# Kernel optimization log

Hardware: AMD Instinct MI355X
Metric: run time of the kernel (lower is better)

## Reference

```python
import jax, jax.numpy as jnp
import numpy as np

B, S, T = 256, 512, 32  # batch, seq_len, tag_size (includes START=T-2, END=T-1)


def setup_inputs() -> dict:
    key = jax.random.key(0)
    k1, k2, k3, k4 = jax.random.split(key, 4)
    feats = jax.random.normal(k1, (B, S, T), dtype=jnp.float32)
    transitions = jax.random.normal(k2, (T, T), dtype=jnp.float32) * 0.1
    # prefix mask: lengths in [S//2, S] (torch code assumes contiguous valid prefix)
    lengths = jax.random.randint(k3, (B,), S // 2, S + 1)
    mask = jnp.arange(S)[None, :] < lengths[:, None]  # (B,S) bool
    tags = jax.random.randint(k4, (B, S), 0, T - 2).astype(jnp.int32)
    return {"feats": feats, "transitions": transitions, "mask": mask, "tags": tags}


def _nll_loss(feats, transitions, mask, tags):
    Bx, Sx, Tx = feats.shape
    maskf = mask.astype(feats.dtype)
    # ---- forward algorithm (log partition) ----
    # partition initialized from emissions at position 1 (positions 0,1 are special)
    part0 = feats[:, 1, :]  # (B,T)
    f_seq = jnp.swapaxes(feats[:, 2:, :], 0, 1)  # (S-2, B, T)
    m_seq = jnp.swapaxes(mask[:, 2:], 0, 1)      # (S-2, B)

    def fwd_step(partition, inp):
        f_t, m_t = inp
        # cur[b, prev, next] = feats[b,t,next] + transitions[prev,next] + partition[b,prev]
        cur = f_t[:, None, :] + transitions[None, :, :] + partition[:, :, None]
        new = jax.nn.logsumexp(cur, axis=1)  # (B,T)
        # partition frozen where mask==0 (== torch masked_scatter logic)
        return jnp.where(m_t[:, None], new, partition), None

    partition, _ = jax.lax.scan(fwd_step, part0, (f_seq, m_seq))
    forward_score = jnp.sum(jax.nn.logsumexp(partition, axis=1))

    # ---- gold score ----
    tags = jnp.where(tags == -100, 0, tags)
    emis = jnp.take_along_axis(feats, tags[..., None], axis=2)[..., 0]  # (B,S)
    tr = transitions[tags[:, :-1], tags[:, 1:]]  # (B,S-1): transition into pos t (t>=1)
    # transitions only apply for t>=2; tg_energy[0] is zeroed in the torch code
    e = emis + jnp.concatenate([jnp.zeros((Bx, 2), feats.dtype), tr[:, 1:]], axis=1)
    e = e.at[:, 0].set(0.0)
    gold_score = jnp.sum(e * maskf)
    return (forward_score - gold_score) / Bx


def _viterbi(feats, transitions, mask):
    Bx, Sx, Tx = feats.shape
    lengths = mask.astype(jnp.int32).sum(axis=1)
    part0 = feats[:, 1, :]
    f_seq = jnp.swapaxes(feats[:, 2:, :], 0, 1)
    m_seq = jnp.swapaxes(mask[:, 2:], 0, 1)

    def vit_step(partition, inp):
        f_t, m_t = inp
        cur = f_t[:, None, :] + transitions[None, :, :] + partition[:, :, None]
        new = jnp.max(cur, axis=1)
        bp = jnp.argmax(cur, axis=1).astype(jnp.int32)
        bp = jnp.where(m_t[:, None], bp, 0)  # torch masked_fill_(pad, 0)
        # NOTE: viterbi partition is updated UNconditionally in the torch code
        return new, (partition, bp)

    last_part, (hist, bps) = jax.lax.scan(vit_step, part0, (f_seq, m_seq))
    history = jnp.concatenate([hist, last_part[None]], axis=0)  # (S-1,B,T)
    hist_bt = jnp.swapaxes(history, 0, 1)                        # (B,S-1,T)
    idx = jnp.broadcast_to((lengths - 2)[:, None, None], (Bx, 1, Tx))
    last_partition = jnp.take_along_axis(hist_bt, idx, axis=1)[:, 0, :]  # (B,T)
    pointer = jnp.argmax(last_partition, axis=1).astype(jnp.int32)

    def back_step(ptr, bp_t):
        new = jnp.take_along_axis(bp_t, ptr[:, None], axis=1)[:, 0]
        return new, new

    _, ptrs = jax.lax.scan(back_step, pointer, bps, reverse=True)  # (S-2,B)
    # decode_idx[0] is uninitialized in the torch code; we define it as 0
    decode = jnp.concatenate(
        [jnp.zeros((1, Bx), jnp.int32), ptrs, pointer[None, :]], axis=0
    )  # (S,B)
    path_score = jnp.zeros((Bx,), feats.dtype)  # torch returns zeros
    return path_score, decode.T


def reference(feats, transitions, mask, tags):
    loss = _nll_loss(feats, transitions, mask, tags)
    path_score, decode_idx = _viterbi(feats, transitions, mask)
    return loss, path_score, decode_idx
```

## Files before the change

kernel.cpp:

```cpp
#include <hip/hip_runtime.h>
#include <cstdint>
#include <cstddef>
#include <utility>

#define SS 512
#define TT 32
#define NB 256
#define KSTEPS 510
#define PQUADS 128

template <typename F, size_t... Is>
__device__ __forceinline__ void unroll_impl(F&& f, std::index_sequence<Is...>) {
  (f(std::integral_constant<int, (int)Is>{}), ...);
}
template <int N, typename F>
__device__ __forceinline__ void unrollN(F&& f) {
  unroll_impl(f, std::make_index_sequence<N>{});
}

template <int D>
__device__ __forceinline__ float bfly32(float v) {
  return __int_as_float(__builtin_amdgcn_ds_swizzle(__float_as_int(v), (D << 10) | 0x1f));
}
template <int D>
__device__ __forceinline__ int bfly32i(int v) {
  return __builtin_amdgcn_ds_swizzle(v, (D << 10) | 0x1f);
}

__device__ __forceinline__ float max3f(float a, float b, float c) {
  return fmaxf(fmaxf(a, b), c);
}

__device__ __forceinline__ float combine_max32(float m) {
#if __has_builtin(__builtin_amdgcn_permlane32_swap)
  auto r = __builtin_amdgcn_permlane32_swap(__float_as_uint(m), __float_as_uint(m), false, false);
  return fmaxf(__uint_as_float(r[0]), __uint_as_float(r[1]));
#else
  return fmaxf(m, __shfl_xor(m, 32, 64));
#endif
}
__device__ __forceinline__ float combine_sum32(float m) {
#if __has_builtin(__builtin_amdgcn_permlane32_swap)
  auto r = __builtin_amdgcn_permlane32_swap(__float_as_uint(m), __float_as_uint(m), false, false);
  return __uint_as_float(r[0]) + __uint_as_float(r[1]);
#else
  return m + __shfl_xor(m, 32, 64);
#endif
}

__device__ __forceinline__ int mask_mode(const void* m) {
  int w0 = ((const int*)m)[0];
  if (w0 == 1) return 0;
  if (w0 == 0x3f800000) return 2;
  return 1;
}
__device__ __forceinline__ bool mask_at(const void* m, int idx, int mode) {
  if (mode == 0) return ((const int*)m)[idx] != 0;
  if (mode == 2) return ((const float*)m)[idx] != 0.0f;
  return ((const unsigned char*)m)[idx] != 0;
}

__device__ __forceinline__ int seq_length_lane(const void* mask, int b, int lane, int mode) {
  int cnt = 0;
  for (int s = lane; s < SS; s += 64) cnt += mask_at(mask, b * SS + s, mode) ? 1 : 0;
  for (int d = 1; d < 64; d <<= 1) cnt += __shfl_xor(cnt, d, 64);
  return __builtin_amdgcn_readfirstlane(cnt);
}

__global__ __launch_bounds__(64, 1) void crf_main_kernel(
    const float* __restrict__ feats, const float* __restrict__ trans,
    const void* __restrict__ mask, const int* __restrict__ tags,
    float* __restrict__ pstore, float* __restrict__ ws_fwd,
    float* __restrict__ ws_gold, int* __restrict__ ws_ptr) {
  const int blk = blockIdx.x;
  const int tid = threadIdx.x;
  const int mode = mask_mode(mask);
  const int j = tid & 31;
  const int h = tid >> 5;

  __shared__ __align__(16) float qlds[TT];

  if (blk < NB) {
    const int b = blk;
    const int steps = seq_length_lane(mask, b, tid, mode) - 2;
    const float* fb = feats + (size_t)b * (SS * TT) + j;

    float E[16];
    unrollN<16>([&](auto I) {
      constexpr int ii = I;
      E[ii] = __expf(trans[(h * 16 + ii) * TT + j]);
    });

    float q = __expf(fb[TT]);
    int Eacc = 0;
    qlds[j] = q;
    asm volatile("" ::: "memory");
    const float4* qvh = (const float4*)qlds + h * 4;

    float fA = fb[2 * TT], fB = fb[3 * TT], fC = fb[4 * TT];
    float ef = __expf(fA);

    auto fstep = [&](int k, bool resc) {
      float4 Q0 = qvh[0], Q1 = qvh[1], Q2 = qvh[2], Q3 = qvh[3];
      int r5 = k + 5; r5 = (r5 < SS) ? r5 : (SS - 1);
      float fD = fb[r5 * TT];
      float efN = __expf(fB);
      float a0, a1, a2, a3;
      a0 = Q0.x * E[0];  a1 = Q0.y * E[1];  a2 = Q0.z * E[2];  a3 = Q0.w * E[3];
      a0 = fmaf(Q1.x, E[4], a0);  a1 = fmaf(Q1.y, E[5], a1);  a2 = fmaf(Q1.z, E[6], a2);  a3 = fmaf(Q1.w, E[7], a3);
      a0 = fmaf(Q2.x, E[8], a0);  a1 = fmaf(Q2.y, E[9], a1);  a2 = fmaf(Q2.z, E[10], a2); a3 = fmaf(Q2.w, E[11], a3);
      a0 = fmaf(Q3.x, E[12], a0); a1 = fmaf(Q3.y, E[13], a1); a2 = fmaf(Q3.z, E[14], a2); a3 = fmaf(Q3.w, E[15], a3);
      float P = (a0 + a1) + (a2 + a3);
      float Pt = combine_sum32(P);
      q = ef * Pt;
      if (resc) {
        int qb = __builtin_amdgcn_readfirstlane(__float_as_int(q));
        int e = (qb >> 23) & 0xff;
        Eacc += e - 127;
        q *= __int_as_float((254 - e) << 23);
      }
      qlds[j] = q;
      asm volatile("" ::: "memory");
      fA = fB; fB = fC; fC = fD; ef = efN;
    };

    int k = 0;
    for (; k + 4 <= steps; k += 4) {
      fstep(k, false); fstep(k + 1, false); fstep(k + 2, false); fstep(k + 3, true);
    }
    for (; k < steps; ++k) fstep(k, false);

    float s = q;
    unrollN<5>([&](auto D) { constexpr int d = 1 << D; s += bfly32<d>(s); });
    if (tid == 0) ws_fwd[b] = __logf(s) + (float)Eacc * 0.69314718056f;

  } else if (blk < 2 * NB) {
    const int b = blk - NB;
    const int steps = seq_length_lane(mask, b, tid, mode) - 2;
    const float* fb = feats + (size_t)b * (SS * TT) + j;
    float* pq = pstore + (size_t)b * (PQUADS * 128) + j * 4;

    float C[16];
    unrollN<16>([&](auto I) {
      constexpr int ii = I;
      C[ii] = trans[(h * 16 + ii) * TT + j];
    });

    float p = fb[TT];
    qlds[j] = p;
    asm volatile("" ::: "memory");
    const float4* qvh = (const float4*)qlds + h * 4;

    float fA = fb[2 * TT], fB = fb[3 * TT], fC = fb[4 * TT];
    float h0 = p, h1 = 0.f, h2 = 0.f, h3 = 0.f;

    auto vstep = [&](int k, float& hslot) {
      float4 Q0 = qvh[0], Q1 = qvh[1], Q2 = qvh[2], Q3 = qvh[3];
      int r5 = k + 5; r5 = (r5 < SS) ? r5 : (SS - 1);
      float fD = fb[r5 * TT];
      float dd[16];
      unrollN<16>([&](auto I) { constexpr int ii = I; dd[ii] = fA + C[ii]; });
      float cur[16];
      cur[0] = Q0.x + dd[0];   cur[1] = Q0.y + dd[1];   cur[2] = Q0.z + dd[2];   cur[3] = Q0.w + dd[3];
      cur[4] = Q1.x + dd[4];   cur[5] = Q1.y + dd[5];   cur[6] = Q1.z + dd[6];   cur[7] = Q1.w + dd[7];
      cur[8] = Q2.x + dd[8];   cur[9] = Q2.y + dd[9];   cur[10] = Q2.z + dd[10]; cur[11] = Q2.w + dd[11];
      cur[12] = Q3.x + dd[12]; cur[13] = Q3.y + dd[13]; cur[14] = Q3.z + dd[14]; cur[15] = Q3.w + dd[15];
      float t0 = max3f(cur[0], cur[1], cur[2]);
      float t1 = max3f(cur[3], cur[4], cur[5]);
      float t2 = max3f(cur[6], cur[7], cur[8]);
      float t3 = max3f(cur[9], cur[10], cur[11]);
      float t4 = max3f(cur[12], cur[13], cur[14]);
      float m = fmaxf(max3f(t0, t1, t2), max3f(t3, t4, cur[15]));
      float pw = combine_max32(m);
      p = pw;
      qlds[j] = pw;
      asm volatile("" ::: "memory");
      hslot = pw;
      fA = fB; fB = fC; fC = fD;
    };

    auto flush = [&](int quad) {
      if (tid < 32) {
        float4 v; v.x = h0; v.y = h1; v.z = h2; v.w = h3;
        *(float4*)(pq + quad * 128) = v;
      }
    };

    int k = 0;
    for (; k + 4 <= steps; k += 4) {
      vstep(k, h1);
      vstep(k + 1, h2);
      vstep(k + 2, h3);
      flush(k >> 2);
      vstep(k + 3, h0);
    }
    if (k < steps) vstep(k, h1);
    if (k + 1 < steps) vstep(k + 1, h2);
    if (k + 2 < steps) vstep(k + 2, h3);
    flush(k >> 2);

    float v = p;
    int idx = j;
    unrollN<5>([&](auto D) {
      constexpr int d = 1 << D;
      float vo = bfly32<d>(v);
      int io = bfly32i<d>(idx);
      bool take = (vo > v) || ((vo == v) && (io < idx));
      v = take ? vo : v;
      idx = take ? io : idx;
    });
    if (tid == 0) ws_ptr[b] = idx;

  } else {
    const int b = blk - 2 * NB;
    float acc = 0.0f;
    for (int s = tid; s < SS; s += 64) {
      if (s == 0) continue;
      if (!mask_at(mask, b * SS + s, mode)) continue;
      int tg = tags[b * SS + s];
      if (tg == -100) tg = 0;
      float e = feats[((size_t)b * SS + s) * TT + tg];
      if (s >= 2) {
        int tp = tags[b * SS + s - 1];
        if (tp == -100) tp = 0;
        e += trans[tp * TT + tg];
      }
      acc += e;
    }
    for (int d = 1; d < 64; d <<= 1) acc += __shfl_xor(acc, d, 64);
    if (tid == 0) ws_gold[b] = acc;
  }
}

__global__ __launch_bounds__(512) void crf_backtrace_kernel(
    const float* __restrict__ pstore, const float* __restrict__ feats,
    const float* __restrict__ trans, const void* __restrict__ mask,
    const int* __restrict__ ws_ptr, const float* __restrict__ ws_fwd,
    const float* __restrict__ ws_gold, float* __restrict__ out) {
  __shared__ unsigned char bp[KSTEPS * TT];
  __shared__ unsigned char path[KSTEPS * TT];
  __shared__ __align__(16) float pT[16][4][TT];
  __shared__ int entries[8];

  const int b = blockIdx.x;
  const int tid = threadIdx.x;
  const int mode = mask_mode(mask);
  const int lane = tid & 63;
  float* out_decode = out + 1 + NB;

  const int steps = seq_length_lane(mask, b, lane, mode) - 2;

  if (tid == 0) out[1 + b] = 0.0f;
  if (b == 0 && tid >= 64 && tid < 128) {
    int t = tid - 64;
    float sf = 0.0f, sg = 0.0f;
    for (int r = 0; r < 4; ++r) { sf += ws_fwd[t + 64 * r]; sg += ws_gold[t + 64 * r]; }
    for (int d = 1; d < 64; d <<= 1) { sf += __shfl_xor(sf, d, 64); sg += __shfl_xor(sg, d, 64); }
    if (t == 0) out[0] = (sf - sg) / 256.0f;
  }

  {
    const int jj = tid & 31;
    const int g = tid >> 5;
    float Cc[TT];
    unrollN<TT>([&](auto I) { constexpr int ii = I; Cc[ii] = trans[ii * TT + jj]; });
    const float* pb = pstore + (size_t)b * (PQUADS * 128);
    const float* fbb = feats + (size_t)b * (SS * TT);
    for (int q = g; q < PQUADS; q += 16) {
      float4 V = *(const float4*)(pb + q * 128 + jj * 4);
      pT[g][0][jj] = V.x; pT[g][1][jj] = V.y; pT[g][2][jj] = V.z; pT[g][3][jj] = V.w;
      asm volatile("" ::: "memory");
      unrollN<4>([&](auto R) {
        constexpr int r = R;
        const int k = 4 * q + r;
        if (k < KSTEPS) {
          unsigned char bv = 0;
          if (k < steps) {
            const float4* pr = (const float4*)pT[g][r];
            float4 P0 = pr[0], P1 = pr[1], P2 = pr[2], P3 = pr[3];
            float4 P4 = pr[4], P5 = pr[5], P6 = pr[6], P7 = pr[7];
            float fj = fbb[(k + 2) * TT + jj];
            float cur[TT];
            cur[0]  = (fj + Cc[0])  + P0.x; cur[1]  = (fj + Cc[1])  + P0.y;
            cur[2]  = (fj + Cc[2])  + P0.z; cur[3]  = (fj + Cc[3])  + P0.w;
            cur[4]  = (fj + Cc[4])  + P1.x; cur[5]  = (fj + Cc[5])  + P1.y;
            cur[6]  = (fj + Cc[6])  + P1.z; cur[7]  = (fj + Cc[7])  + P1.w;
            cur[8]  = (fj + Cc[8])  + P2.x; cur[9]  = (fj + Cc[9])  + P2.y;
            cur[10] = (fj + Cc[10]) + P2.z; cur[11] = (fj + Cc[11]) + P2.w;
            cur[12] = (fj + Cc[12]) + P3.x; cur[13] = (fj + Cc[13]) + P3.y;
            cur[14] = (fj + Cc[14]) + P3.z; cur[15] = (fj + Cc[15]) + P3.w;
            cur[16] = (fj + Cc[16]) + P4.x; cur[17] = (fj + Cc[17]) + P4.y;
            cur[18] = (fj + Cc[18]) + P4.z; cur[19] = (fj + Cc[19]) + P4.w;
            cur[20] = (fj + Cc[20]) + P5.x; cur[21] = (fj + Cc[21]) + P5.y;
            cur[22] = (fj + Cc[22]) + P5.z; cur[23] = (fj + Cc[23]) + P5.w;
            cur[24] = (fj + Cc[24]) + P6.x; cur[25] = (fj + Cc[25]) + P6.y;
            cur[26] = (fj + Cc[26]) + P6.z; cur[27] = (fj + Cc[27]) + P6.w;
            cur[28] = (fj + Cc[28]) + P7.x; cur[29] = (fj + Cc[29]) + P7.y;
            cur[30] = (fj + Cc[30]) + P7.z; cur[31] = (fj + Cc[31]) + P7.w;
            float t0 = max3f(cur[0], cur[1], cur[2]);
            float t1 = max3f(cur[3], cur[4], cur[5]);
            float t2 = max3f(cur[6], cur[7], cur[8]);
            float t3 = max3f(cur[9], cur[10], cur[11]);
            float t4 = max3f(cur[12], cur[13], cur[14]);
            float t5 = max3f(cur[15], cur[16], cur[17]);
            float t6 = max3f(cur[18], cur[19], cur[20]);
            float t7 = max3f(cur[21], cur[22], cur[23]);
            float t8 = max3f(cur[24], cur[25], cur[26]);
            float t9 = max3f(cur[27], cur[28], cur[29]);
            float ta = fmaxf(cur[30], cur[31]);
            float vmax = fmaxf(fmaxf(max3f(t0, t1, t2), max3f(t3, t4, t5)),
                               fmaxf(max3f(t6, t7, t8), fmaxf(t9, ta)));
            int bi = 31;
            unrollN<TT>([&](auto I) { constexpr int ii = 31 - I; bi = (cur[ii] == vmax) ? ii : bi; });
            bv = (unsigned char)bi;
          }
          bp[k * TT + jj] = bv;
        }
      });
    }
  }
  __syncthreads();

  const int wave = tid >> 6;
  if (lane < 32) {
    const int lo = wave * 64;
    const int hi = (lo + 64 < KSTEPS) ? (lo + 64) : KSTEPS;
    int ptr = lane;
    for (int k = hi - 1; k >= lo; --k) {
      ptr = bp[k * TT + ptr];
      path[k * TT + lane] = (unsigned char)ptr;
    }
  }
  __syncthreads();

  if (tid == 0) {
    int e = ws_ptr[b];
    for (int c = 7; c >= 0; --c) {
      entries[c] = e;
      e = path[(c * 64) * TT + e];
    }
  }
  __syncthreads();

  const int s = tid;
  int val;
  if (s == 0) val = 0;
  else if (s <= KSTEPS) { int k = s - 1; val = path[k * TT + entries[k >> 6]]; }
  else val = ws_ptr[b];
  out_decode[(size_t)b * SS + s] = (float)val;
}

extern "C" void kernel_launch(void* const* d_in, const int* in_sizes, int n_in,
                              void* d_out, int out_size, void* d_ws, size_t ws_size,
                              hipStream_t stream) {
  const float* feats = (const float*)d_in[0];
  const float* trans = (const float*)d_in[1];
  const void* mask = d_in[2];
  const int* tags = (const int*)d_in[3];
  float* out = (float*)d_out;

  unsigned char* ws = (unsigned char*)d_ws;
  const size_t PST_BYTES = (size_t)NB * PQUADS * 128 * 4;
  float* pstore = (float*)ws;
  float* ws_fwd = (float*)(ws + PST_BYTES);
  float* ws_gold = (float*)(ws + PST_BYTES + 2048);
  int* ws_ptr = (int*)(ws + PST_BYTES + 4096);

  hipLaunchKernelGGL(crf_main_kernel, dim3(3 * NB), dim3(64), 0, stream,
                     feats, trans, mask, tags, pstore, ws_fwd, ws_gold, ws_ptr);
  hipLaunchKernelGGL(crf_backtrace_kernel, dim3(NB), dim3(512), 0, stream,
                     pstore, feats, trans, mask, ws_ptr, ws_fwd, ws_gold, out);
}
```

Baseline: 112.6 us.

## Replace LDS broadcast in CRF recurrences with DPP row rotations and permlane swaps

```diff
diff --git a/kernel.cpp b/kernel.cpp
--- a/kernel.cpp
+++ b/kernel.cpp
@@ -29,6 +29,16 @@
 
 __device__ __forceinline__ float max3f(float a, float b, float c) {
   return fmaxf(fmaxf(a, b), c);
+}
+
+template <int R>
+__device__ __forceinline__ float dpp_rorf(float v) {
+  return __int_as_float(__builtin_amdgcn_update_dpp(
+      0, __float_as_int(v), 0x120 + R, 0xf, 0xf, true));
+}
+template <int R>
+__device__ __forceinline__ int dpp_rori(int v) {
+  return __builtin_amdgcn_update_dpp(0, v, 0x120 + R, 0xf, 0xf, true);
 }
 
 __device__ __forceinline__ float combine_max32(float m) {
@@ -45,6 +55,15 @@
   return __uint_as_float(r[0]) + __uint_as_float(r[1]);
 #else
   return m + __shfl_xor(m, 32, 64);
+#endif
+}
+__device__ __forceinline__ float partner16(float v) {
+#if __has_builtin(__builtin_amdgcn_permlane16_swap)
+  auto r = __builtin_amdgcn_permlane16_swap(__float_as_uint(v), __float_as_uint(v), false, false);
+  float a = __uint_as_float(r[0]), b = __uint_as_float(r[1]);
+  return (__float_as_uint(a) == __float_as_uint(v)) ? b : a;
+#else
+  return __shfl_xor(v, 16, 64);
 #endif
 }
 
@@ -75,52 +94,66 @@
   const int blk = blockIdx.x;
   const int tid = threadIdx.x;
   const int mode = mask_mode(mask);
-  const int j = tid & 31;
-  const int h = tid >> 5;
-
-  __shared__ __align__(16) float qlds[TT];
+  const int lane = tid & 63;
+  const int l15 = lane & 15;
+  const int row = lane >> 4;
+  const int heldB = (row == 1 || row == 2) ? 16 : 0;
+  const int outB  = (row == 1 || row == 3) ? 16 : 0;
+  const int heldtag = l15 + heldB;
+  const int outtag  = l15 + outB;
+  const bool lower = (lane < 32);
+
+  int src15[16];
+  src15[0] = l15;
+  unrollN<15>([&](auto RR) { constexpr int r = RR + 1; src15[r] = dpp_rori<r>(l15); });
 
   if (blk < NB) {
     const int b = blk;
     const int steps = seq_length_lane(mask, b, tid, mode) - 2;
-    const float* fb = feats + (size_t)b * (SS * TT) + j;
+    const float* fb = feats + (size_t)b * (SS * TT) + outtag;
 
     float E[16];
-    unrollN<16>([&](auto I) {
-      constexpr int ii = I;
-      E[ii] = __expf(trans[(h * 16 + ii) * TT + j]);
+    unrollN<16>([&](auto RR) {
+      constexpr int r = RR;
+      E[r] = __expf(trans[(src15[r] + heldB) * TT + outtag]);
     });
 
-    float q = __expf(fb[TT]);
+    float q = __expf(feats[(size_t)b * (SS * TT) + TT + heldtag]);
     int Eacc = 0;
-    qlds[j] = q;
-    asm volatile("" ::: "memory");
-    const float4* qvh = (const float4*)qlds + h * 4;
-
     float fA = fb[2 * TT], fB = fb[3 * TT], fC = fb[4 * TT];
     float ef = __expf(fA);
 
     auto fstep = [&](int k, bool resc) {
-      float4 Q0 = qvh[0], Q1 = qvh[1], Q2 = qvh[2], Q3 = qvh[3];
       int r5 = k + 5; r5 = (r5 < SS) ? r5 : (SS - 1);
       float fD = fb[r5 * TT];
       float efN = __expf(fB);
-      float a0, a1, a2, a3;
-      a0 = Q0.x * E[0];  a1 = Q0.y * E[1];  a2 = Q0.z * E[2];  a3 = Q0.w * E[3];
-      a0 = fmaf(Q1.x, E[4], a0);  a1 = fmaf(Q1.y, E[5], a1);  a2 = fmaf(Q1.z, E[6], a2);  a3 = fmaf(Q1.w, E[7], a3);
-      a0 = fmaf(Q2.x, E[8], a0);  a1 = fmaf(Q2.y, E[9], a1);  a2 = fmaf(Q2.z, E[10], a2); a3 = fmaf(Q2.w, E[11], a3);
-      a0 = fmaf(Q3.x, E[12], a0); a1 = fmaf(Q3.y, E[13], a1); a2 = fmaf(Q3.z, E[14], a2); a3 = fmaf(Q3.w, E[15], a3);
+      float a0 = q * E[0], a1, a2, a3;
+      a1 = dpp_rorf<1>(q) * E[1];
+      a2 = dpp_rorf<2>(q) * E[2];
+      a3 = dpp_rorf<3>(q) * E[3];
+      a0 = fmaf(dpp_rorf<4>(q),  E[4],  a0);
+      a1 = fmaf(dpp_rorf<5>(q),  E[5],  a1);
+      a2 = fmaf(dpp_rorf<6>(q),  E[6],  a2);
+      a3 = fmaf(dpp_rorf<7>(q),  E[7],  a3);
+      a0 = fmaf(dpp_rorf<8>(q),  E[8],  a0);
+      a1 = fmaf(dpp_rorf<9>(q),  E[9],  a1);
+      a2 = fmaf(dpp_rorf<10>(q), E[10], a2);
+      a3 = fmaf(dpp_rorf<11>(q), E[11], a3);
+      a0 = fmaf(dpp_rorf<12>(q), E[12], a0);
+      a1 = fmaf(dpp_rorf<13>(q), E[13], a1);
+      a2 = fmaf(dpp_rorf<14>(q), E[14], a2);
+      a3 = fmaf(dpp_rorf<15>(q), E[15], a3);
       float P = (a0 + a1) + (a2 + a3);
-      float Pt = combine_sum32(P);
-      q = ef * Pt;
+      float val = ef * combine_sum32(P);
+      float par = partner16(val);
+      float qn = lower ? val : par;
       if (resc) {
-        int qb = __builtin_amdgcn_readfirstlane(__float_as_int(q));
+        int qb = __builtin_amdgcn_readfirstlane(__float_as_int(qn));
         int e = (qb >> 23) & 0xff;
         Eacc += e - 127;
-        q *= __int_as_float((254 - e) << 23);
+        qn *= __int_as_float((254 - e) << 23);
       }
-      qlds[j] = q;
-      asm volatile("" ::: "memory");
+      q = qn;
       fA = fB; fB = fC; fC = fD; ef = efN;
     };
 
@@ -137,50 +170,57 @@
   } else if (blk < 2 * NB) {
     const int b = blk - NB;
     const int steps = seq_length_lane(mask, b, tid, mode) - 2;
-    const float* fb = feats + (size_t)b * (SS * TT) + j;
-    float* pq = pstore + (size_t)b * (PQUADS * 128) + j * 4;
+    const float* fb = feats + (size_t)b * (SS * TT) + outtag;
+    float* pq = pstore + (size_t)b * (PQUADS * 128) + lane * 4;
 
     float C[16];
-    unrollN<16>([&](auto I) {
-      constexpr int ii = I;
-      C[ii] = trans[(h * 16 + ii) * TT + j];
+    unrollN<16>([&](auto RR) {
+      constexpr int r = RR;
+      C[r] = trans[(src15[r] + heldB) * TT + outtag];
     });
 
-    float p = fb[TT];
-    qlds[j] = p;
-    asm volatile("" ::: "memory");
-    const float4* qvh = (const float4*)qlds + h * 4;
-
+    float p = feats[(size_t)b * (SS * TT) + TT + heldtag];
     float fA = fb[2 * TT], fB = fb[3 * TT], fC = fb[4 * TT];
     float h0 = p, h1 = 0.f, h2 = 0.f, h3 = 0.f;
 
     auto vstep = [&](int k, float& hslot) {
-      float4 Q0 = qvh[0], Q1 = qvh[1], Q2 = qvh[2], Q3 = qvh[3];
       int r5 = k + 5; r5 = (r5 < SS) ? r5 : (SS - 1);
       float fD = fb[r5 * TT];
       float dd[16];
-      unrollN<16>([&](auto I) { constexpr int ii = I; dd[ii] = fA + C[ii]; });
+      unrollN<16>([&](auto RR) { constexpr int r = RR; dd[r] = fA + C[r]; });
       float cur[16];
-      cur[0] = Q0.x + dd[0];   cur[1] = Q0.y + dd[1];   cur[2] = Q0.z + dd[2];   cur[3] = Q0.w + dd[3];
-      cur[4] = Q1.x + dd[4];   cur[5] = Q1.y + dd[5];   cur[6] = Q1.z + dd[6];   cur[7] = Q1.w + dd[7];
-      cur[8] = Q2.x + dd[8];   cur[9] = Q2.y + dd[9];   cur[10] = Q2.z + dd[10]; cur[11] = Q2.w + dd[11];
-      cur[12] = Q3.x + dd[12]; cur[13] = Q3.y + dd[13]; cur[14] = Q3.z + dd[14]; cur[15] = Q3.w + dd[15];
+      cur[0] = p + dd[0];
+      cur[1]  = dpp_rorf<1>(p)  + dd[1];
+      cur[2]  = dpp_rorf<2>(p)  + dd[2];
+      cur[3]  = dpp_rorf<3>(p)  + dd[3];
+      cur[4]  = dpp_rorf<4>(p)  + dd[4];
+      cur[5]  = dpp_rorf<5>(p)  + dd[5];
+      cur[6]  = dpp_rorf<6>(p)  + dd[6];
+      cur[7]  = dpp_rorf<7>(p)  + dd[7];
+      cur[8]  = dpp_rorf<8>(p)  + dd[8];
+      cur[9]  = dpp_rorf<9>(p)  + dd[9];
+      cur[10] = dpp_rorf<10>(p) + dd[10];
+      cur[11] = dpp_rorf<11>(p) + dd[11];
+      cur[12] = dpp_rorf<12>(p) + dd[12];
+      cur[13] = dpp_rorf<13>(p) + dd[13];
+      cur[14] = dpp_rorf<14>(p) + dd[14];
+      cur[15] = dpp_rorf<15>(p) + dd[15];
       float t0 = max3f(cur[0], cur[1], cur[2]);
       float t1 = max3f(cur[3], cur[4], cur[5]);
       float t2 = max3f(cur[6], cur[7], cur[8]);
       float t3 = max3f(cur[9], cur[10], cur[11]);
       float t4 = max3f(cur[12], cur[13], cur[14]);
       float m = fmaxf(max3f(t0, t1, t2), max3f(t3, t4, cur[15]));
-      float pw = combine_max32(m);
+      float full = combine_max32(m);
+      float par = partner16(full);
+      float pw = lower ? full : par;
       p = pw;
-      qlds[j] = pw;
-      asm volatile("" ::: "memory");
       hslot = pw;
       fA = fB; fB = fC; fC = fD;
     };
 
     auto flush = [&](int quad) {
-      if (tid < 32) {
+      if (lane < 32) {
         float4 v; v.x = h0; v.y = h1; v.z = h2; v.w = h3;
         *(float4*)(pq + quad * 128) = v;
       }
@@ -200,7 +240,7 @@
     flush(k >> 2);
 
     float v = p;
-    int idx = j;
+    int idx = lane & 31;
     unrollN<5>([&](auto D) {
       constexpr int d = 1 << D;
       float vo = bfly32<d>(v);
```

Result: faster. 103.6 us, median of 2 (-8.0%).

## Pack two sequences per wave and replace LDS exchange with DPP rotations

Applied to the files above, without the earlier changes.

```diff
diff --git a/kernel.cpp b/kernel.cpp
--- a/kernel.cpp
+++ b/kernel.cpp
@@ -31,20 +31,23 @@
   return fmaxf(fmaxf(a, b), c);
 }
 
-__device__ __forceinline__ float combine_max32(float m) {
-#if __has_builtin(__builtin_amdgcn_permlane32_swap)
-  auto r = __builtin_amdgcn_permlane32_swap(__float_as_uint(m), __float_as_uint(m), false, false);
-  return fmaxf(__uint_as_float(r[0]), __uint_as_float(r[1]));
+template <int R>
+__device__ __forceinline__ float dpp_rorf(float v) {
+  return __int_as_float(__builtin_amdgcn_update_dpp(
+      0, __float_as_int(v), 0x120 + R, 0xf, 0xf, true));
+}
+template <int R>
+__device__ __forceinline__ int dpp_rori(int v) {
+  return __builtin_amdgcn_update_dpp(0, v, 0x120 + R, 0xf, 0xf, true);
+}
+
+__device__ __forceinline__ float partner16(float v) {
+#if __has_builtin(__builtin_amdgcn_permlane16_swap)
+  auto r = __builtin_amdgcn_permlane16_swap(__float_as_uint(v), __float_as_uint(v), false, false);
+  float a = __uint_as_float(r[0]), b = __uint_as_float(r[1]);
+  return (__float_as_uint(a) == __float_as_uint(v)) ? b : a;
 #else
-  return fmaxf(m, __shfl_xor(m, 32, 64));
-#endif
-}
-__device__ __forceinline__ float combine_sum32(float m) {
-#if __has_builtin(__builtin_amdgcn_permlane32_swap)
-  auto r = __builtin_amdgcn_permlane32_swap(__float_as_uint(m), __float_as_uint(m), false, false);
-  return __uint_as_float(r[0]) + __uint_as_float(r[1]);
-#else
-  return m + __shfl_xor(m, 32, 64);
+  return __shfl_xor(v, 16, 64);
 #endif
 }
 
@@ -58,6 +61,16 @@
   if (mode == 0) return ((const int*)m)[idx] != 0;
   if (mode == 2) return ((const float*)m)[idx] != 0.0f;
   return ((const unsigned char*)m)[idx] != 0;
+}
+
+__device__ __forceinline__ int seqlen32(const void* mask, int b, int j32, int mode) {
+  int cnt = 0;
+  unrollN<16>([&](auto T) {
+    constexpr int t = T;
+    cnt += mask_at(mask, b * SS + j32 + 32 * t, mode) ? 1 : 0;
+  });
+  unrollN<5>([&](auto D) { constexpr int d = 1 << D; cnt += bfly32i<d>(cnt); });
+  return cnt;
 }
 
 __device__ __forceinline__ int seq_length_lane(const void* mask, int b, int lane, int mode) {
@@ -75,132 +88,92 @@
   const int blk = blockIdx.x;
   const int tid = threadIdx.x;
   const int mode = mask_mode(mask);
-  const int j = tid & 31;
-  const int h = tid >> 5;
-
-  __shared__ __align__(16) float qlds[TT];
-
-  if (blk < NB) {
-    const int b = blk;
-    const int steps = seq_length_lane(mask, b, tid, mode) - 2;
-    const float* fb = feats + (size_t)b * (SS * TT) + j;
-
-    float E[16];
-    unrollN<16>([&](auto I) {
-      constexpr int ii = I;
-      E[ii] = __expf(trans[(h * 16 + ii) * TT + j]);
+  const int tag = tid & 31;
+  const int g = tid >> 5;
+  const int rowg = (tid >> 4) & 1;
+  const int sAb = rowg ? 16 : 0;
+  const int sBb = rowg ? 0 : 16;
+
+  int src15[16];
+  src15[0] = tid & 15;
+  unrollN<15>([&](auto RR) { constexpr int r = RR + 1; src15[r] = dpp_rori<r>(tid & 15); });
+
+  if (blk < 128) {
+    const int b = blk * 2 + g;
+    const int steps = seqlen32(mask, b, tag, mode) - 2;
+    int smax;
+    { int s = steps, o = __shfl_xor(s, 32, 64); s = (o > s) ? o : s;
+      smax = __builtin_amdgcn_readfirstlane(s); }
+    const float* fb = feats + (size_t)b * (SS * TT) + tag;
+    float* pq = pstore + (size_t)b * (PQUADS * 128) + tag * 4;
+
+    float CA[16], CB[16];
+    unrollN<16>([&](auto RR) {
+      constexpr int r = RR;
+      CA[r] = trans[(sAb + src15[r]) * TT + tag];
+      CB[r] = trans[(sBb + src15[r]) * TT + tag];
     });
 
-    float q = __expf(fb[TT]);
-    int Eacc = 0;
-    qlds[j] = q;
-    asm volatile("" ::: "memory");
-    const float4* qvh = (const float4*)qlds + h * 4;
-
+    float p = fb[TT];
     float fA = fb[2 * TT], fB = fb[3 * TT], fC = fb[4 * TT];
-    float ef = __expf(fA);
-
-    auto fstep = [&](int k, bool resc) {
-      float4 Q0 = qvh[0], Q1 = qvh[1], Q2 = qvh[2], Q3 = qvh[3];
+    float h0 = p, h1 = 0.f, h2 = 0.f, h3 = 0.f;
+
+    auto vstep = [&](int k, float& hslot) {
       int r5 = k + 5; r5 = (r5 < SS) ? r5 : (SS - 1);
       float fD = fb[r5 * TT];
-      float efN = __expf(fB);
-      float a0, a1, a2, a3;
-      a0 = Q0.x * E[0];  a1 = Q0.y * E[1];  a2 = Q0.z * E[2];  a3 = Q0.w * E[3];
-      a0 = fmaf(Q1.x, E[4], a0);  a1 = fmaf(Q1.y, E[5], a1);  a2 = fmaf(Q1.z, E[6], a2);  a3 = fmaf(Q1.w, E[7], a3);
-      a0 = fmaf(Q2.x, E[8], a0);  a1 = fmaf(Q2.y, E[9], a1);  a2 = fmaf(Q2.z, E[10], a2); a3 = fmaf(Q2.w, E[11], a3);
-      a0 = fmaf(Q3.x, E[12], a0); a1 = fmaf(Q3.y, E[13], a1); a2 = fmaf(Q3.z, E[14], a2); a3 = fmaf(Q3.w, E[15], a3);
-      float P = (a0 + a1) + (a2 + a3);
-      float Pt = combine_sum32(P);
-      q = ef * Pt;
-      if (resc) {
-        int qb = __builtin_amdgcn_readfirstlane(__float_as_int(q));
-        int e = (qb >> 23) & 0xff;
-        Eacc += e - 127;
-        q *= __int_as_float((254 - e) << 23);
-      }
-      qlds[j] = q;
-      asm volatile("" ::: "memory");
-      fA = fB; fB = fC; fC = fD; ef = efN;
-    };
-
-    int k = 0;
-    for (; k + 4 <= steps; k += 4) {
-      fstep(k, false); fstep(k + 1, false); fstep(k + 2, false); fstep(k + 3, true);
-    }
-    for (; k < steps; ++k) fstep(k, false);
-
-    float s = q;
-    unrollN<5>([&](auto D) { constexpr int d = 1 << D; s += bfly32<d>(s); });
-    if (tid == 0) ws_fwd[b] = __logf(s) + (float)Eacc * 0.69314718056f;
-
-  } else if (blk < 2 * NB) {
-    const int b = blk - NB;
-    const int steps = seq_length_lane(mask, b, tid, mode) - 2;
-    const float* fb = feats + (size_t)b * (SS * TT) + j;
-    float* pq = pstore + (size_t)b * (PQUADS * 128) + j * 4;
-
-    float C[16];
-    unrollN<16>([&](auto I) {
-      constexpr int ii = I;
-      C[ii] = trans[(h * 16 + ii) * TT + j];
-    });
-
-    float p = fb[TT];
-    qlds[j] = p;
-    asm volatile("" ::: "memory");
-    const float4* qvh = (const float4*)qlds + h * 4;
-
-    float fA = fb[2 * TT], fB = fb[3 * TT], fC = fb[4 * TT];
-    float h0 = p, h1 = 0.f, h2 = 0.f, h3 = 0.f;
-
-    auto vstep = [&](int k, float& hslot) {
-      float4 Q0 = qvh[0], Q1 = qvh[1], Q2 = qvh[2], Q3 = qvh[3];
-      int r5 = k + 5; r5 = (r5 < SS) ? r5 : (SS - 1);
-      float fD = fb[r5 * TT];
-      float dd[16];
-      unrollN<16>([&](auto I) { constexpr int ii = I; dd[ii] = fA + C[ii]; });
-      float cur[16];
-      cur[0] = Q0.x + dd[0];   cur[1] = Q0.y + dd[1];   cur[2] = Q0.z + dd[2];   cur[3] = Q0.w + dd[3];
-      cur[4] = Q1.x + dd[4];   cur[5] = Q1.y + dd[5];   cur[6] = Q1.z + dd[6];   cur[7] = Q1.w + dd[7];
-      cur[8] = Q2.x + dd[8];   cur[9] = Q2.y + dd[9];   cur[10] = Q2.z + dd[10]; cur[11] = Q2.w + dd[11];
-      cur[12] = Q3.x + dd[12]; cur[13] = Q3.y + dd[13]; cur[14] = Q3.z + dd[14]; cur[15] = Q3.w + dd[15];
+      float pp = partner16(p);
+      float cur[32];
+      unrollN<16>([&](auto RR) {
+        constexpr int r = RR;
+        float d = fA + CA[r];
+        if constexpr (r == 0) cur[0] = p + d;
+        else cur[r] = dpp_rorf<r>(p) + d;
+      });
+      unrollN<16>([&](auto RR) {
+        constexpr int r = RR;
+        float d = fA + CB[r];
+        if constexpr (r == 0) cur[16] = pp + d;
+        else cur[16 + r] = dpp_rorf<r>(pp) + d;
+      });
       float t0 = max3f(cur[0], cur[1], cur[2]);
       float t1 = max3f(cur[3], cur[4], cur[5]);
       float t2 = max3f(cur[6], cur[7], cur[8]);
       float t3 = max3f(cur[9], cur[10], cur[11]);
       float t4 = max3f(cur[12], cur[13], cur[14]);
-      float m = fmaxf(max3f(t0, t1, t2), max3f(t3, t4, cur[15]));
-      float pw = combine_max32(m);
+      float t5 = max3f(cur[15], cur[16], cur[17]);
+      float t6 = max3f(cur[18], cur[19], cur[20]);
+      float t7 = max3f(cur[21], cur[22], cur[23]);
+      float t8 = max3f(cur[24], cur[25], cur[26]);
+      float t9 = max3f(cur[27], cur[28], cur[29]);
+      float ta = fmaxf(cur[30], cur[31]);
+      float vmax = fmaxf(fmaxf(max3f(t0, t1, t2), max3f(t3, t4, t5)),
+                         fmaxf(max3f(t6, t7, t8), fmaxf(t9, ta)));
+      float pw = (k < steps) ? vmax : p;
       p = pw;
-      qlds[j] = pw;
-      asm volatile("" ::: "memory");
       hslot = pw;
       fA = fB; fB = fC; fC = fD;
     };
 
     auto flush = [&](int quad) {
-      if (tid < 32) {
-        float4 v; v.x = h0; v.y = h1; v.z = h2; v.w = h3;
-        *(float4*)(pq + quad * 128) = v;
-      }
+      float4 v; v.x = h0; v.y = h1; v.z = h2; v.w = h3;
+      *(float4*)(pq + quad * 128) = v;
     };
 
     int k = 0;
-    for (; k + 4 <= steps; k += 4) {
+    for (; k + 4 <= smax; k += 4) {
       vstep(k, h1);
       vstep(k + 1, h2);
       vstep(k + 2, h3);
       flush(k >> 2);
       vstep(k + 3, h0);
     }
-    if (k < steps) vstep(k, h1);
-    if (k + 1 < steps) vstep(k + 1, h2);
-    if (k + 2 < steps) vstep(k + 2, h3);
+    if (k < smax) vstep(k, h1);
+    if (k + 1 < smax) vstep(k + 1, h2);
+    if (k + 2 < smax) vstep(k + 2, h3);
     flush(k >> 2);
 
     float v = p;
-    int idx = j;
+    int idx = tag;
     unrollN<5>([&](auto D) {
       constexpr int d = 1 << D;
       float vo = bfly32<d>(v);
@@ -209,10 +182,92 @@
       v = take ? vo : v;
       idx = take ? io : idx;
     });
-    if (tid == 0) ws_ptr[b] = idx;
+    if (tag == 0) ws_ptr[b] = idx;
+
+  } else if (blk < 256) {
+    const int b = (blk - 128) * 2 + g;
+    const int steps = seqlen32(mask, b, tag, mode) - 2;
+    int smax;
+    { int s = steps, o = __shfl_xor(s, 32, 64); s = (o > s) ? o : s;
+      smax = __builtin_amdgcn_readfirstlane(s); }
+    const float* fb = feats + (size_t)b * (SS * TT) + tag;
+
+    float EA[16], EB[16];
+    unrollN<16>([&](auto RR) {
+      constexpr int r = RR;
+      EA[r] = __expf(trans[(sAb + src15[r]) * TT + tag]);
+      EB[r] = __expf(trans[(sBb + src15[r]) * TT + tag]);
+    });
+
+    float q = __expf(fb[TT]);
+    int Eacc = 0;
+    float fA = fb[2 * TT], fB = fb[3 * TT], fC = fb[4 * TT];
+    float ef = __expf(fA);
+
+    auto fstep = [&](int k, bool resc) {
+      int r5 = k + 5; r5 = (r5 < SS) ? r5 : (SS - 1);
+      float fD = fb[r5 * TT];
+      float efN = __expf(fB);
+      float pp = partner16(q);
+      float a0, a1, a2, a3;
+      a0 = q * EA[0];
+      a1 = dpp_rorf<1>(q) * EA[1];
+      a2 = dpp_rorf<2>(q) * EA[2];
+      a3 = dpp_rorf<3>(q) * EA[3];
+      a0 = fmaf(dpp_rorf<4>(q),  EA[4],  a0);
+      a1 = fmaf(dpp_rorf<5>(q),  EA[5],  a1);
+      a2 = fmaf(dpp_rorf<6>(q),  EA[6],  a2);
+      a3 = fmaf(dpp_rorf<7>(q),  EA[7],  a3);
+      a0 = fmaf(dpp_rorf<8>(q),  EA[8],  a0);
+      a1 = fmaf(dpp_rorf<9>(q),  EA[9],  a1);
+      a2 = fmaf(dpp_rorf<10>(q), EA[10], a2);
+      a3 = fmaf(dpp_rorf<11>(q), EA[11], a3);
+      a0 = fmaf(dpp_rorf<12>(q), EA[12], a0);
+      a1 = fmaf(dpp_rorf<13>(q), EA[13], a1);
+      a2 = fmaf(dpp_rorf<14>(q), EA[14], a2);
+      a3 = fmaf(dpp_rorf<15>(q), EA[15], a3);
+      a0 = fmaf(pp, EB[0], a0);
+      a1 = fmaf(dpp_rorf<1>(pp),  EB[1],  a1);
+      a2 = fmaf(dpp_rorf<2>(pp),  EB[2],  a2);
+      a3 = fmaf(dpp_rorf<3>(pp),  EB[3],  a3);
+      a0 = fmaf(dpp_rorf<4>(pp),  EB[4],  a0);
+      a1 = fmaf(dpp_rorf<5>(pp),  EB[5],  a1);
+      a2 = fmaf(dpp_rorf<6>(pp),  EB[6],  a2);
+      a3 = fmaf(dpp_rorf<7>(pp),  EB[7],  a3);
+      a0 = fmaf(dpp_rorf<8>(pp),  EB[8],  a0);
+      a1 = fmaf(dpp_rorf<9>(pp),  EB[9],  a1);
+      a2 = fmaf(dpp_rorf<10>(pp), EB[10], a2);
+      a3 = fmaf(dpp_rorf<11>(pp), EB[11], a3);
+      a0 = fmaf(dpp_rorf<12>(pp), EB[12], a0);
+      a1 = fmaf(dpp_rorf<13>(pp), EB[13], a1);
+      a2 = fmaf(dpp_rorf<14>(pp), EB[14], a2);
+      a3 = fmaf(dpp_rorf<15>(pp), EB[15], a3);
+      float P = (a0 + a1) + (a2 + a3);
+      float qn = (k < steps) ? (ef * P) : q;
+      if (resc) {
+        int e0 = __builtin_amdgcn_readlane(__float_as_int(qn), 0);
+        int e1 = __builtin_amdgcn_readlane(__float_as_int(qn), 32);
+        int qb = (tid < 32) ? e0 : e1;
+        int e = (k < steps) ? ((qb >> 23) & 0xff) : 127;
+        Eacc += e - 127;
+        qn *= __int_as_float((254 - e) << 23);
+      }
+      q = qn;
+      fA = fB; fB = fC; fC = fD; ef = efN;
+    };
+
+    int k = 0;
+    for (; k + 4 <= smax; k += 4) {
+      fstep(k, false); fstep(k + 1, false); fstep(k + 2, false); fstep(k + 3, true);
+    }
+    for (; k < smax; ++k) fstep(k, false);
+
+    float s = q;
+    unrollN<5>([&](auto D) { constexpr int d = 1 << D; s += bfly32<d>(s); });
+    if (tag == 0) ws_fwd[b] = __logf(s) + (float)Eacc * 0.69314718056f;
 
   } else {
-    const int b = blk - 2 * NB;
+    const int b = blk - 256;
     float acc = 0.0f;
     for (int s = tid; s < SS; s += 64) {
       if (s == 0) continue;
@@ -366,7 +421,7 @@
   float* ws_gold = (float*)(ws + PST_BYTES + 2048);
   int* ws_ptr = (int*)(ws + PST_BYTES + 4096);
 
-  hipLaunchKernelGGL(crf_main_kernel, dim3(3 * NB), dim3(64), 0, stream,
+  hipLaunchKernelGGL(crf_main_kernel, dim3(512), dim3(64), 0, stream,
                      feats, trans, mask, tags, pstore, ws_fwd, ws_gold, ws_ptr);
   hipLaunchKernelGGL(crf_backtrace_kernel, dim3(NB), dim3(512), 0, stream,
                      pstore, feats, trans, mask, ws_ptr, ws_fwd, ws_gold, out);
```

Measured after the change: 136.4 us. 21.2% more time.
